# Performance work log

Hardware: AMD Instinct MI355X
Metric: run time of the kernel (lower is better)

## Reference

```python
import jax, jax.numpy as jnp
import numpy as np
from functools import partial

ITERS = 100
EPSILON = 0.8
TAU = 1.02
FEATURE_DIM = 256
MATCHED_THRESHOLD = 0.2
B, D, N0, N1 = 1, 256, 2048, 2048


def log_optimal_transport_extended(scores, alpha, iters, epsilon, tau):
    b, m, n = scores.shape
    dt = scores.dtype
    ms = jnp.asarray(m, dt)
    ns = jnp.asarray(n, dt)
    bins0 = jnp.broadcast_to(alpha, (b, m, 1)).astype(dt)
    bins1 = jnp.broadcast_to(alpha, (b, 1, n)).astype(dt)
    corner = jnp.broadcast_to(alpha, (b, 1, 1)).astype(dt)
    # couplings: [b, m+1, n+1] score matrix augmented with dustbin row/col
    couplings = jnp.concatenate([
        jnp.concatenate([scores, bins0], axis=-1),
        jnp.concatenate([bins1, corner], axis=-1)], axis=1)
    norm = -jnp.log(ms + ns)
    log_mu = jnp.concatenate([jnp.full((m,), norm, dt), (jnp.log(ns) + norm)[None]])
    log_nu = jnp.concatenate([jnp.full((n,), norm, dt), (jnp.log(ms) + norm)[None]])
    log_mu = jnp.broadcast_to(log_mu[None], (b, m + 1))
    log_nu = jnp.broadcast_to(log_nu[None], (b, n + 1))

    def step(carry, _):
        u, v = carry
        u_new = (log_mu - jax.scipy.special.logsumexp(couplings + v[:, None, :], axis=2)) / tau
        u = u + epsilon * (u_new - u)
        v_new = (log_nu - jax.scipy.special.logsumexp(couplings + u[:, :, None], axis=1)) / tau
        v = v + epsilon * (v_new - v)
        return (u, v), None

    u0 = jnp.zeros_like(log_mu)
    v0 = jnp.zeros_like(log_nu)
    (u, v), _ = jax.lax.scan(jax.checkpoint(step), (u0, v0), None, length=iters)
    Z = couplings + u[:, :, None] + v[:, None, :]
    return Z - norm


def reference(mdesc0, mdesc1, bin_score):
    # mdesc0: [b, d, n], mdesc1: [b, d, m]
    sim = jnp.einsum('bdn,bdm->bnm', mdesc0, mdesc1)
    scores = sim / np.float32(np.sqrt(FEATURE_DIM))
    Z = log_optimal_transport_extended(scores, bin_score, ITERS, EPSILON, TAU)
    inner = Z[:, :-1, :-1]                       # [b, m, n]
    m, n = inner.shape[1], inner.shape[2]
    max0_vals = inner.max(axis=2)
    indices0 = inner.argmax(axis=2)              # [b, m] int
    indices1 = inner.argmax(axis=1)              # [b, n] int
    mutual0 = jnp.arange(m)[None, :] == jnp.take_along_axis(indices1, indices0, axis=1)
    mutual1 = jnp.arange(n)[None, :] == jnp.take_along_axis(indices0, indices1, axis=1)
    zero = jnp.zeros((), inner.dtype)
    mscores0 = jnp.where(mutual0, jnp.exp(max0_vals), zero)
    mscores1 = jnp.where(mutual1, jnp.take_along_axis(mscores0, indices1, axis=1), zero)
    valid0 = mutual0 & (mscores0 > MATCHED_THRESHOLD)
    valid1 = mutual1 & jnp.take_along_axis(valid0, indices1, axis=1)
    i0 = jnp.where(valid0, indices0, -1)
    i1 = jnp.where(valid1, indices1, -1)
    return (jnp.exp(Z[0]), i0[0], i1[0], mscores0[0], mscores1[0])


def setup_inputs() -> dict:
    key = jax.random.key(0)
    k0, k1 = jax.random.split(key)
    mdesc0 = jax.random.normal(k0, (B, D, N0), dtype=jnp.float32)
    mdesc1 = jax.random.normal(k1, (B, D, N1), dtype=jnp.float32)
    bin_score = jnp.ones((), dtype=jnp.float32)  # learned dustbin score, init 1.0
    return {"mdesc0": mdesc0, "mdesc1": mdesc1, "bin_score": bin_score}
```

## Files before the change

kernel.cpp:

```cpp
#include <hip/hip_runtime.h>
#include <hip/hip_bf16.h>
#include <math.h>

#define D        256
#define NINNER   2048
#define NROW     2049
#define SP       2064
#define ITERS_N  100
#define EPS_F    0.8f
#define TAU_F    1.02f
#define NB       256
#define NT       256

typedef unsigned long long u64;

#define PSTRIDE  2112u

#define SZ_MAT   (2049u * 2064u)
#define OFF_E    0u
#define OFF_F    SZ_MAT
#define OFF_WUP  (2u * SZ_MAT)
#define OFF_WVP  (OFF_WUP + 4u * PSTRIDE)
#define OFF_MAX0 (OFF_WVP + 4u * PSTRIDE)
#define OFF_IDX0 (OFF_MAX0 + 2048u)
#define OFF_IDX1 (OFF_IDX0 + 2048u)
#define OFF_MS0  (OFF_IDX1 + 2048u)
#define OFF_VLD0 (OFF_MS0 + 2048u)

#define OOFF_Z   0u
#define OOFF_I0  (2049u * 2049u)
#define OOFF_I1  (OOFF_I0 + 2048u)
#define OOFF_S0  (OOFF_I1 + 2048u)
#define OOFF_S1  (OOFF_S0 + 2048u)

__device__ __forceinline__ float    pair_val(u64 x) { return __uint_as_float((unsigned)x); }
__device__ __forceinline__ unsigned pair_tag(u64 x) { return (unsigned)(x >> 32); }
__device__ __forceinline__ u64 make_pair(float v, unsigned t) {
    return ((u64)t << 32) | (u64)__float_as_uint(v);
}

__global__ __launch_bounds__(256) void k_gemm(const float* __restrict__ A,
                                              const float* __restrict__ Bm,
                                              float* __restrict__ E,
                                              float* __restrict__ F) {
    __shared__ float As[8][64];
    __shared__ float Bs[8][64];
    const int tid = threadIdx.x;
    const int tx = tid & 15, ty = tid >> 4;
    const int row0 = blockIdx.y * 64, col0 = blockIdx.x * 64;
    float acc[4][4] = {};
    const int lr = tid >> 6, lc = tid & 63;
    for (int k0 = 0; k0 < D; k0 += 8) {
        As[lr][lc]     = A[(k0 + lr) * NINNER + row0 + lc];
        As[lr + 4][lc] = A[(k0 + lr + 4) * NINNER + row0 + lc];
        Bs[lr][lc]     = Bm[(k0 + lr) * NINNER + col0 + lc];
        Bs[lr + 4][lc] = Bm[(k0 + lr + 4) * NINNER + col0 + lc];
        __syncthreads();
#pragma unroll
        for (int kk = 0; kk < 8; ++kk) {
            const float4 av = *(const float4*)&As[kk][ty * 4];
            const float4 bv = *(const float4*)&Bs[kk][tx * 4];
            const float a_[4] = {av.x, av.y, av.z, av.w};
            const float b_[4] = {bv.x, bv.y, bv.z, bv.w};
#pragma unroll
            for (int r = 0; r < 4; ++r)
#pragma unroll
                for (int c = 0; c < 4; ++c)
                    acc[r][c] = fmaf(a_[r], b_[c], acc[r][c]);
        }
        __syncthreads();
    }
    float o[4][4];
#pragma unroll
    for (int r = 0; r < 4; ++r)
#pragma unroll
        for (int c = 0; c < 4; ++c)
            o[r][c] = expf(acc[r][c] * 0.0625f);
    const int row = row0 + ty * 4, col = col0 + tx * 4;
#pragma unroll
    for (int r = 0; r < 4; ++r)
        *(float4*)(E + (size_t)(row + r) * SP + col)
            = make_float4(o[r][0], o[r][1], o[r][2], o[r][3]);
#pragma unroll
    for (int c = 0; c < 4; ++c)
        *(float4*)(F + (size_t)(col + c) * SP + row)
            = make_float4(o[0][c], o[1][c], o[2][c], o[3][c]);
}

__global__ __launch_bounds__(256) void k_init(float* __restrict__ E,
                                              float* __restrict__ F,
                                              u64* __restrict__ wvb0,
                                              const float* __restrict__ alpha) {
    const int t = blockIdx.x * 256 + threadIdx.x;
    const float ea = expf(alpha[0]);
    if (t < NINNER) {
        E[(size_t)t * SP + NINNER] = ea;
        F[(size_t)t * SP + NINNER] = ea;
        wvb0[t] = make_pair(1.0f, 0u);
    }
    if (t <= NINNER) {
        E[(size_t)NINNER * SP + t] = ea;
        F[(size_t)NINNER * SP + t] = ea;
    }
}

__device__ __forceinline__ void poll8(const u64* buf, int tid, unsigned want, float* w) {
    u64 a[8];
#pragma unroll
    for (int q = 0; q < 8; ++q)
        a[q] = __hip_atomic_load(buf + q * 256 + tid, __ATOMIC_RELAXED, __HIP_MEMORY_SCOPE_AGENT);
    for (;;) {
        unsigned miss = 0u;
#pragma unroll
        for (int q = 0; q < 8; ++q)
            miss |= (pair_tag(a[q]) != want) ? (1u << q) : 0u;
        if (!miss) break;
        __builtin_amdgcn_s_sleep(2);
#pragma unroll
        for (int q = 0; q < 8; ++q)
            if (miss & (1u << q))
                a[q] = __hip_atomic_load(buf + q * 256 + tid, __ATOMIC_RELAXED, __HIP_MEMORY_SCOPE_AGENT);
    }
#pragma unroll
    for (int q = 0; q < 8; ++q) w[q] = pair_val(a[q]);
}

__global__ __launch_bounds__(256, 1) void k_sinkhorn(const float* __restrict__ E,
                                                     const float* __restrict__ F,
                                                     u64* wub, u64* wvb,
                                                     const float* __restrict__ alpha) {
    const int b = blockIdx.x, tid = threadIdx.x;
    const int lane = tid & 63, wid = tid >> 6;
    const int base = b * 8;
    const bool lastb = (b == NB - 1);
    __shared__ float red[2][4][9];

    const float norm = -8.317766166719343f;
    const float logbin = 7.624618986159398f + norm;
    const float ea = expf(alpha[0]);

    float eR[8][8], fR[8][8];
#pragma unroll
    for (int r = 0; r < 8; ++r) {
        const float* rowE = E + (size_t)(base + r) * SP;
        const float* rowF = F + (size_t)(base + r) * SP;
#pragma unroll
        for (int q = 0; q < 8; ++q) {
            eR[r][q] = rowE[q * 256 + tid];
            fR[r][q] = rowF[q * 256 + tid];
        }
    }

    float u = 0.0f, v = 0.0f;
    float ub = 0.0f, vb = 0.0f;
    float eub = 1.0f, evb = 1.0f;

    for (int it = 0; it < ITERS_N; ++it) {
        {
            const u64* src = wvb + (size_t)(it & 1) * PSTRIDE;
            u64* dst = wub + (size_t)((it + 1) & 1) * PSTRIDE;
            const unsigned prod = (unsigned)(it + 1);
            float w[8];
            poll8(src, tid, (unsigned)it, w);
            float p[8];
#pragma unroll
            for (int r = 0; r < 8; ++r) {
                float s = 0.0f;
#pragma unroll
                for (int q = 0; q < 8; ++q) s = fmaf(eR[r][q], w[q], s);
                p[r] = s;
            }
            float t = w[0] + w[1] + w[2] + w[3] + w[4] + w[5] + w[6] + w[7];
#pragma unroll
            for (int r = 0; r < 8; ++r) {
                float s = p[r];
#pragma unroll
                for (int m = 1; m < 64; m <<= 1) s += __shfl_xor(s, m, 64);
                if (lane == 0) red[0][wid][r] = s;
            }
#pragma unroll
            for (int m = 1; m < 64; m <<= 1) t += __shfl_xor(t, m, 64);
            if (lane == 0) red[0][wid][8] = t;
            __syncthreads();
            const float tsum = red[0][0][8] + red[0][1][8] + red[0][2][8] + red[0][3][8];
            const float Sbin = ea * (tsum + evb);
            ub = ub + EPS_F * ((logbin - logf(Sbin)) / TAU_F - ub);
            if (tid < 8) {
                const float S = red[0][0][tid] + red[0][1][tid] + red[0][2][tid] + red[0][3][tid]
                              + ea * evb;
                const float unew = (norm - logf(S)) / TAU_F;
                u = u + EPS_F * (unew - u);
                __hip_atomic_store(dst + base + tid, make_pair(expf(u), prod),
                                   __ATOMIC_RELAXED, __HIP_MEMORY_SCOPE_AGENT);
            }
            eub = expf(ub);
        }
        {
            const u64* src = wub + (size_t)((it + 1) & 1) * PSTRIDE;
            u64* dst = wvb + (size_t)((it + 1) & 1) * PSTRIDE;
            const unsigned prod = (unsigned)(it + 1);
            float w[8];
            poll8(src, tid, prod, w);
            float p[8];
#pragma unroll
            for (int r = 0; r < 8; ++r) {
                float s = 0.0f;
#pragma unroll
                for (int q = 0; q < 8; ++q) s = fmaf(fR[r][q], w[q], s);
                p[r] = s;
            }
            float t = w[0] + w[1] + w[2] + w[3] + w[4] + w[5] + w[6] + w[7];
#pragma unroll
            for (int r = 0; r < 8; ++r) {
                float s = p[r];
#pragma unroll
                for (int m = 1; m < 64; m <<= 1) s += __shfl_xor(s, m, 64);
                if (lane == 0) red[1][wid][r] = s;
            }
#pragma unroll
            for (int m = 1; m < 64; m <<= 1) t += __shfl_xor(t, m, 64);
            if (lane == 0) red[1][wid][8] = t;
            __syncthreads();
            const float tsum = red[1][0][8] + red[1][1][8] + red[1][2][8] + red[1][3][8];
            const float Tbin = ea * (tsum + eub);
            vb = vb + EPS_F * ((logbin - logf(Tbin)) / TAU_F - vb);
            if (tid < 8) {
                const float T = red[1][0][tid] + red[1][1][tid] + red[1][2][tid] + red[1][3][tid]
                              + ea * eub;
                const float vnew = (norm - logf(T)) / TAU_F;
                v = v + EPS_F * (vnew - v);
                __hip_atomic_store(dst + base + tid, make_pair(expf(v), prod),
                                   __ATOMIC_RELAXED, __HIP_MEMORY_SCOPE_AGENT);
            }
            evb = expf(vb);
        }
    }
    if (lastb && tid == 0) {
        __hip_atomic_store(wub + NINNER, make_pair(eub, (unsigned)ITERS_N),
                           __ATOMIC_RELAXED, __HIP_MEMORY_SCOPE_AGENT);
        __hip_atomic_store(wvb + NINNER, make_pair(evb, (unsigned)ITERS_N),
                           __ATOMIC_RELAXED, __HIP_MEMORY_SCOPE_AGENT);
    }
}

__global__ __launch_bounds__(256) void k_finish(const float* __restrict__ E,
                                                const float* __restrict__ F,
                                                const float2* __restrict__ wup,
                                                const float2* __restrict__ wvp,
                                                float* __restrict__ out,
                                                float* __restrict__ max0,
                                                int* __restrict__ idx0,
                                                int* __restrict__ idx1) {
    const int i = blockIdx.x;
    const int tid = threadIdx.x;
    const int lane = tid & 63, wid = tid >> 6;
    __shared__ float sb[4]; __shared__ int si[4];

    {
        const float wui = wup[i].x * 4096.0f;
        const float* row = E + (size_t)i * SP;
        float best = -1.0f; int bidx = 0;
        for (int j = tid; j < NROW; j += 256) {
            const float val = row[j] * wvp[j].x * wui;
            out[(size_t)i * NROW + j] = val;
            if (j < NINNER && val > best) { best = val; bidx = j; }
        }
        if (i < NINNER) {
#pragma unroll
            for (int m = 1; m < 64; m <<= 1) {
                const float ob = __shfl_xor(best, m, 64);
                const int   oi = __shfl_xor(bidx, m, 64);
                if (ob > best || (ob == best && oi < bidx)) { best = ob; bidx = oi; }
            }
            if (lane == 0) { sb[wid] = best; si[wid] = bidx; }
            __syncthreads();
            if (tid == 0) {
                for (int k = 1; k < 4; ++k)
                    if (sb[k] > best || (sb[k] == best && si[k] < bidx)) { best = sb[k]; bidx = si[k]; }
                max0[i] = best; idx0[i] = bidx;
            }
        }
    }

    if (i < NINNER) {
        __syncthreads();
        const float* row = F + (size_t)i * SP;
        float best = -1.0f; int bidx = 0;
        for (int r = tid; r < NINNER; r += 256) {
            const float q = row[r] * wup[r].x;
            if (q > best) { best = q; bidx = r; }
        }
#pragma unroll
        for (int m = 1; m < 64; m <<= 1) {
            const float ob = __shfl_xor(best, m, 64);
            const int   oi = __shfl_xor(bidx, m, 64);
            if (ob > best || (ob == best && oi < bidx)) { best = ob; bidx = oi; }
        }
        if (lane == 0) { sb[wid] = best; si[wid] = bidx; }
        __syncthreads();
        if (tid == 0) {
            for (int k = 1; k < 4; ++k)
                if (sb[k] > best || (sb[k] == best && si[k] < bidx)) { best = sb[k]; bidx = si[k]; }
            idx1[i] = bidx;
        }
    }
}

__global__ __launch_bounds__(256) void k_match0(const float* __restrict__ max0,
                                                const int* __restrict__ idx0,
                                                const int* __restrict__ idx1,
                                                float* __restrict__ ms0,
                                                int* __restrict__ vld0,
                                                float* __restrict__ out) {
    const int i = blockIdx.x * 256 + threadIdx.x;
    if (i >= NINNER) return;
    const int j = idx0[i];
    const bool mut = (idx1[j] == i);
    const float ms = mut ? max0[i] : 0.0f;
    const bool val = mut && (ms > 0.2f);
    ms0[i] = ms; vld0[i] = val ? 1 : 0;
    out[OOFF_I0 + i] = val ? (float)j : -1.0f;
    out[OOFF_S0 + i] = ms;
}
__global__ __launch_bounds__(256) void k_match1(const int* __restrict__ idx0,
                                                const int* __restrict__ idx1,
                                                const float* __restrict__ ms0,
                                                const int* __restrict__ vld0,
                                                float* __restrict__ out) {
    const int j = blockIdx.x * 256 + threadIdx.x;
    if (j >= NINNER) return;
    const int i = idx1[j];
    const bool mut = (idx0[i] == j);
    const float ms = mut ? ms0[i] : 0.0f;
    const bool val = mut && (vld0[i] != 0);
    out[OOFF_I1 + j] = val ? (float)i : -1.0f;
    out[OOFF_S1 + j] = ms;
}

extern "C" void kernel_launch(void* const* d_in, const int* in_sizes, int n_in,
                              void* d_out, int out_size, void* d_ws, size_t ws_size,
                              hipStream_t stream) {
    const float* A     = (const float*)d_in[0];
    const float* Bm    = (const float*)d_in[1];
    const float* alpha = (const float*)d_in[2];

    float* ws = (float*)d_ws;
    float* E    = ws + OFF_E;
    float* F    = ws + OFF_F;
    u64*   wub  = (u64*)(ws + OFF_WUP);
    u64*   wvb  = (u64*)(ws + OFF_WVP);
    float* max0 = ws + OFF_MAX0;
    int*   idx0 = (int*)(ws + OFF_IDX0);
    int*   idx1 = (int*)(ws + OFF_IDX1);
    float* ms0  = ws + OFF_MS0;
    int*   vld0 = (int*)(ws + OFF_VLD0);
    float* out  = (float*)d_out;

    k_gemm<<<dim3(32, 32), 256, 0, stream>>>(A, Bm, E, F);
    k_init<<<dim3(16), 256, 0, stream>>>(E, F, wvb, alpha);
    k_sinkhorn<<<dim3(NB), NT, 0, stream>>>(E, F, wub, wvb, alpha);
    k_finish<<<dim3(NROW), 256, 0, stream>>>(E, F, (const float2*)wub, (const float2*)wvb,
                                             out, max0, idx0, idx1);
    k_match0<<<dim3(8), 256, 0, stream>>>(max0, idx0, idx1, ms0, vld0, out);
    k_match1<<<dim3(8), 256, 0, stream>>>(idx0, idx1, ms0, vld0, out);
}
```

Before: 901.4 us.

## Replace tagged per-element flag polling with sharded atomic counter barriers

```diff
diff --git a/kernel.cpp b/kernel.cpp
--- a/kernel.cpp
+++ b/kernel.cpp
@@ -1,5 +1,4 @@
 #include <hip/hip_runtime.h>
-#include <hip/hip_bf16.h>
 #include <math.h>
 
 #define D        256
@@ -12,32 +11,23 @@
 #define NB       256
 #define NT       256
 
-typedef unsigned long long u64;
-
-#define PSTRIDE  2112u
-
 #define SZ_MAT   (2049u * 2064u)
 #define OFF_E    0u
 #define OFF_F    SZ_MAT
-#define OFF_WUP  (2u * SZ_MAT)
-#define OFF_WVP  (OFF_WUP + 4u * PSTRIDE)
-#define OFF_MAX0 (OFF_WVP + 4u * PSTRIDE)
+#define OFF_WU   (2u * SZ_MAT)
+#define OFF_WV   (OFF_WU + 2064u)
+#define OFF_CU   (OFF_WV + 2064u)
+#define OFF_CV   (OFF_CU + 512u)
+#define OFF_MAX0 (OFF_CV + 512u)
 #define OFF_IDX0 (OFF_MAX0 + 2048u)
 #define OFF_IDX1 (OFF_IDX0 + 2048u)
 #define OFF_MS0  (OFF_IDX1 + 2048u)
 #define OFF_VLD0 (OFF_MS0 + 2048u)
 
-#define OOFF_Z   0u
 #define OOFF_I0  (2049u * 2049u)
 #define OOFF_I1  (OOFF_I0 + 2048u)
 #define OOFF_S0  (OOFF_I1 + 2048u)
 #define OOFF_S1  (OOFF_S0 + 2048u)
-
-__device__ __forceinline__ float    pair_val(u64 x) { return __uint_as_float((unsigned)x); }
-__device__ __forceinline__ unsigned pair_tag(u64 x) { return (unsigned)(x >> 32); }
-__device__ __forceinline__ u64 make_pair(float v, unsigned t) {
-    return ((u64)t << 32) | (u64)__float_as_uint(v);
-}
 
 __global__ __launch_bounds__(256) void k_gemm(const float* __restrict__ A,
                                               const float* __restrict__ Bm,
@@ -89,50 +79,37 @@
 
 __global__ __launch_bounds__(256) void k_init(float* __restrict__ E,
                                               float* __restrict__ F,
-                                              u64* __restrict__ wvb0,
+                                              float* __restrict__ wv,
+                                              unsigned* __restrict__ cu,
+                                              unsigned* __restrict__ cv,
                                               const float* __restrict__ alpha) {
     const int t = blockIdx.x * 256 + threadIdx.x;
     const float ea = expf(alpha[0]);
     if (t < NINNER) {
         E[(size_t)t * SP + NINNER] = ea;
         F[(size_t)t * SP + NINNER] = ea;
-        wvb0[t] = make_pair(1.0f, 0u);
+        wv[t] = 1.0f;
     }
     if (t <= NINNER) {
         E[(size_t)NINNER * SP + t] = ea;
         F[(size_t)NINNER * SP + t] = ea;
     }
-}
-
-__device__ __forceinline__ void poll8(const u64* buf, int tid, unsigned want, float* w) {
-    u64 a[8];
-#pragma unroll
-    for (int q = 0; q < 8; ++q)
-        a[q] = __hip_atomic_load(buf + q * 256 + tid, __ATOMIC_RELAXED, __HIP_MEMORY_SCOPE_AGENT);
-    for (;;) {
-        unsigned miss = 0u;
-#pragma unroll
-        for (int q = 0; q < 8; ++q)
-            miss |= (pair_tag(a[q]) != want) ? (1u << q) : 0u;
-        if (!miss) break;
-        __builtin_amdgcn_s_sleep(2);
-#pragma unroll
-        for (int q = 0; q < 8; ++q)
-            if (miss & (1u << q))
-                a[q] = __hip_atomic_load(buf + q * 256 + tid, __ATOMIC_RELAXED, __HIP_MEMORY_SCOPE_AGENT);
-    }
-#pragma unroll
-    for (int q = 0; q < 8; ++q) w[q] = pair_val(a[q]);
+    if (t < 8) {
+        cu[t * 64] = 0u;
+        cv[t * 64] = NB / 8;
+    }
 }
 
 __global__ __launch_bounds__(256, 1) void k_sinkhorn(const float* __restrict__ E,
                                                      const float* __restrict__ F,
-                                                     u64* wub, u64* wvb,
+                                                     float* __restrict__ wu,
+                                                     float* __restrict__ wv,
+                                                     unsigned* __restrict__ cu,
+                                                     unsigned* __restrict__ cv,
                                                      const float* __restrict__ alpha) {
     const int b = blockIdx.x, tid = threadIdx.x;
     const int lane = tid & 63, wid = tid >> 6;
     const int base = b * 8;
-    const bool lastb = (b == NB - 1);
     __shared__ float red[2][4][9];
 
     const float norm = -8.317766166719343f;
@@ -156,12 +133,25 @@
     float eub = 1.0f, evb = 1.0f;
 
     for (int it = 0; it < ITERS_N; ++it) {
+        const unsigned tgt = (unsigned)(NB * (it + 1));
         {
-            const u64* src = wvb + (size_t)(it & 1) * PSTRIDE;
-            u64* dst = wub + (size_t)((it + 1) & 1) * PSTRIDE;
-            const unsigned prod = (unsigned)(it + 1);
+            if (tid == 0) {
+                for (;;) {
+                    unsigned s = 0;
+#pragma unroll
+                    for (int k = 0; k < 8; ++k)
+                        s += __hip_atomic_load(cv + k * 64, __ATOMIC_RELAXED,
+                                               __HIP_MEMORY_SCOPE_AGENT);
+                    if (s >= tgt) break;
+                    __builtin_amdgcn_s_sleep(1);
+                }
+            }
+            __syncthreads();
             float w[8];
-            poll8(src, tid, (unsigned)it, w);
+#pragma unroll
+            for (int q = 0; q < 8; ++q)
+                w[q] = __hip_atomic_load(wv + q * 256 + tid, __ATOMIC_RELAXED,
+                                         __HIP_MEMORY_SCOPE_AGENT);
             float p[8];
 #pragma unroll
             for (int r = 0; r < 8; ++r) {
@@ -190,17 +180,32 @@
                               + ea * evb;
                 const float unew = (norm - logf(S)) / TAU_F;
                 u = u + EPS_F * (unew - u);
-                __hip_atomic_store(dst + base + tid, make_pair(expf(u), prod),
+                __hip_atomic_store(wu + base + tid, expf(u),
                                    __ATOMIC_RELAXED, __HIP_MEMORY_SCOPE_AGENT);
             }
+            if (tid == 0)
+                __hip_atomic_fetch_add(cu + (b & 7) * 64, 1u,
+                                       __ATOMIC_RELEASE, __HIP_MEMORY_SCOPE_AGENT);
             eub = expf(ub);
         }
         {
-            const u64* src = wub + (size_t)((it + 1) & 1) * PSTRIDE;
-            u64* dst = wvb + (size_t)((it + 1) & 1) * PSTRIDE;
-            const unsigned prod = (unsigned)(it + 1);
+            if (tid == 0) {
+                for (;;) {
+                    unsigned s = 0;
+#pragma unroll
+                    for (int k = 0; k < 8; ++k)
+                        s += __hip_atomic_load(cu + k * 64, __ATOMIC_RELAXED,
+                                               __HIP_MEMORY_SCOPE_AGENT);
+                    if (s >= tgt) break;
+                    __builtin_amdgcn_s_sleep(1);
+                }
+            }
+            __syncthreads();
             float w[8];
-            poll8(src, tid, prod, w);
+#pragma unroll
+            for (int q = 0; q < 8; ++q)
+                w[q] = __hip_atomic_load(wu + q * 256 + tid, __ATOMIC_RELAXED,
+                                         __HIP_MEMORY_SCOPE_AGENT);
             float p[8];
 #pragma unroll
             for (int r = 0; r < 8; ++r) {
@@ -229,24 +234,25 @@
                               + ea * eub;
                 const float vnew = (norm - logf(T)) / TAU_F;
                 v = v + EPS_F * (vnew - v);
-                __hip_atomic_store(dst + base + tid, make_pair(expf(v), prod),
+                __hip_atomic_store(wv + base + tid, expf(v),
                                    __ATOMIC_RELAXED, __HIP_MEMORY_SCOPE_AGENT);
             }
+            if (tid == 0)
+                __hip_atomic_fetch_add(cv + (b & 7) * 64, 1u,
+                                       __ATOMIC_RELEASE, __HIP_MEMORY_SCOPE_AGENT);
             evb = expf(vb);
         }
     }
-    if (lastb && tid == 0) {
-        __hip_atomic_store(wub + NINNER, make_pair(eub, (unsigned)ITERS_N),
-                           __ATOMIC_RELAXED, __HIP_MEMORY_SCOPE_AGENT);
-        __hip_atomic_store(wvb + NINNER, make_pair(evb, (unsigned)ITERS_N),
-                           __ATOMIC_RELAXED, __HIP_MEMORY_SCOPE_AGENT);
+    if (b == NB - 1 && tid == 0) {
+        wu[NINNER] = eub;
+        wv[NINNER] = evb;
     }
 }
 
 __global__ __launch_bounds__(256) void k_finish(const float* __restrict__ E,
                                                 const float* __restrict__ F,
-                                                const float2* __restrict__ wup,
-                                                const float2* __restrict__ wvp,
+                                                const float* __restrict__ wu,
+                                                const float* __restrict__ wv,
                                                 float* __restrict__ out,
                                                 float* __restrict__ max0,
                                                 int* __restrict__ idx0,
@@ -257,11 +263,11 @@
     __shared__ float sb[4]; __shared__ int si[4];
 
     {
-        const float wui = wup[i].x * 4096.0f;
+        const float wui = wu[i] * 4096.0f;
         const float* row = E + (size_t)i * SP;
         float best = -1.0f; int bidx = 0;
         for (int j = tid; j < NROW; j += 256) {
-            const float val = row[j] * wvp[j].x * wui;
+            const float val = row[j] * wv[j] * wui;
             out[(size_t)i * NROW + j] = val;
             if (j < NINNER && val > best) { best = val; bidx = j; }
         }
@@ -287,7 +293,7 @@
         const float* row = F + (size_t)i * SP;
         float best = -1.0f; int bidx = 0;
         for (int r = tid; r < NINNER; r += 256) {
-            const float q = row[r] * wup[r].x;
+            const float q = row[r] * wu[r];
             if (q > best) { best = q; bidx = r; }
         }
 #pragma unroll
@@ -345,22 +351,23 @@
     const float* alpha = (const float*)d_in[2];
 
     float* ws = (float*)d_ws;
-    float* E    = ws + OFF_E;
-    float* F    = ws + OFF_F;
-    u64*   wub  = (u64*)(ws + OFF_WUP);
-    u64*   wvb  = (u64*)(ws + OFF_WVP);
-    float* max0 = ws + OFF_MAX0;
-    int*   idx0 = (int*)(ws + OFF_IDX0);
-    int*   idx1 = (int*)(ws + OFF_IDX1);
-    float* ms0  = ws + OFF_MS0;
-    int*   vld0 = (int*)(ws + OFF_VLD0);
-    float* out  = (float*)d_out;
+    float* E      = ws + OFF_E;
+    float* F      = ws + OFF_F;
+    float* wu     = ws + OFF_WU;
+    float* wv     = ws + OFF_WV;
+    unsigned* cu  = (unsigned*)(ws + OFF_CU);
+    unsigned* cv  = (unsigned*)(ws + OFF_CV);
+    float* max0   = ws + OFF_MAX0;
+    int*   idx0   = (int*)(ws + OFF_IDX0);
+    int*   idx1   = (int*)(ws + OFF_IDX1);
+    float* ms0    = ws + OFF_MS0;
+    int*   vld0   = (int*)(ws + OFF_VLD0);
+    float* out    = (float*)d_out;
 
     k_gemm<<<dim3(32, 32), 256, 0, stream>>>(A, Bm, E, F);
-    k_init<<<dim3(16), 256, 0, stream>>>(E, F, wvb, alpha);
-    k_sinkhorn<<<dim3(NB), NT, 0, stream>>>(E, F, wub, wvb, alpha);
-    k_finish<<<dim3(NROW), 256, 0, stream>>>(E, F, (const float2*)wub, (const float2*)wvb,
-                                             out, max0, idx0, idx1);
+    k_init<<<dim3(16), 256, 0, stream>>>(E, F, wv, cu, cv, alpha);
+    k_sinkhorn<<<dim3(NB), NT, 0, stream>>>(E, F, wu, wv, cu, cv, alpha);
+    k_finish<<<dim3(NROW), 256, 0, stream>>>(E, F, wu, wv, out, max0, idx0, idx1);
     k_match0<<<dim3(8), 256, 0, stream>>>(max0, idx0, idx1, ms0, vld0, out);
     k_match1<<<dim3(8), 256, 0, stream>>>(idx0, idx1, ms0, vld0, out);
 }
```

Measured after the change: 1.244 ms. +38.0%, slower.

## Halve Sinkhorn block count with 16 rows per block and vectorized polling

Applied to the files above, without the earlier changes.

```diff
diff --git a/kernel.cpp b/kernel.cpp
--- a/kernel.cpp
+++ b/kernel.cpp
@@ -1,5 +1,4 @@
 #include <hip/hip_runtime.h>
-#include <hip/hip_bf16.h>
 #include <math.h>
 
 #define D        256
@@ -9,10 +8,12 @@
 #define ITERS_N  100
 #define EPS_F    0.8f
 #define TAU_F    1.02f
-#define NB       256
-#define NT       256
+#define NB_S     128
+#define NT_S     512
+#define ROWS     16
 
 typedef unsigned long long u64;
+typedef __attribute__((ext_vector_type(4))) unsigned int uint4v;
 
 #define PSTRIDE  2112u
 
@@ -27,7 +28,6 @@
 #define OFF_MS0  (OFF_IDX1 + 2048u)
 #define OFF_VLD0 (OFF_MS0 + 2048u)
 
-#define OOFF_Z   0u
 #define OOFF_I0  (2049u * 2049u)
 #define OOFF_I1  (OOFF_I0 + 2048u)
 #define OOFF_S0  (OOFF_I1 + 2048u)
@@ -104,51 +104,45 @@
     }
 }
 
-__device__ __forceinline__ void poll8(const u64* buf, int tid, unsigned want, float* w) {
-    u64 a[8];
-#pragma unroll
-    for (int q = 0; q < 8; ++q)
-        a[q] = __hip_atomic_load(buf + q * 256 + tid, __ATOMIC_RELAXED, __HIP_MEMORY_SCOPE_AGENT);
+__device__ __forceinline__ void poll4(const u64* buf, int tid, unsigned want, float* w) {
+    const u64* p = buf + 4 * (size_t)tid;
+    uint4v x, y;
     for (;;) {
-        unsigned miss = 0u;
-#pragma unroll
-        for (int q = 0; q < 8; ++q)
-            miss |= (pair_tag(a[q]) != want) ? (1u << q) : 0u;
-        if (!miss) break;
-        __builtin_amdgcn_s_sleep(2);
-#pragma unroll
-        for (int q = 0; q < 8; ++q)
-            if (miss & (1u << q))
-                a[q] = __hip_atomic_load(buf + q * 256 + tid, __ATOMIC_RELAXED, __HIP_MEMORY_SCOPE_AGENT);
-    }
-#pragma unroll
-    for (int q = 0; q < 8; ++q) w[q] = pair_val(a[q]);
-}
-
-__global__ __launch_bounds__(256, 1) void k_sinkhorn(const float* __restrict__ E,
+        asm volatile("global_load_dwordx4 %0, %2, off sc0 sc1\n\t"
+                     "global_load_dwordx4 %1, %2, off offset:16 sc0 sc1\n\t"
+                     "s_waitcnt vmcnt(0)"
+                     : "=&v"(x), "=&v"(y)
+                     : "v"(p)
+                     : "memory");
+        if (x.y == want && x.w == want && y.y == want && y.w == want) break;
+        __builtin_amdgcn_s_sleep(1);
+    }
+    __builtin_amdgcn_sched_barrier(0);
+    w[0] = __uint_as_float(x.x); w[1] = __uint_as_float(x.z);
+    w[2] = __uint_as_float(y.x); w[3] = __uint_as_float(y.z);
+}
+
+__global__ __launch_bounds__(512, 2) void k_sinkhorn(const float* __restrict__ E,
                                                      const float* __restrict__ F,
                                                      u64* wub, u64* wvb,
                                                      const float* __restrict__ alpha) {
     const int b = blockIdx.x, tid = threadIdx.x;
     const int lane = tid & 63, wid = tid >> 6;
-    const int base = b * 8;
-    const bool lastb = (b == NB - 1);
-    __shared__ float red[2][4][9];
+    const int base = b * ROWS;
+    const bool lastb = (b == NB_S - 1);
+    __shared__ float red[2][8][17];
 
     const float norm = -8.317766166719343f;
     const float logbin = 7.624618986159398f + norm;
     const float ea = expf(alpha[0]);
 
-    float eR[8][8], fR[8][8];
-#pragma unroll
-    for (int r = 0; r < 8; ++r) {
-        const float* rowE = E + (size_t)(base + r) * SP;
-        const float* rowF = F + (size_t)(base + r) * SP;
-#pragma unroll
-        for (int q = 0; q < 8; ++q) {
-            eR[r][q] = rowE[q * 256 + tid];
-            fR[r][q] = rowF[q * 256 + tid];
-        }
+    float eR[ROWS][4], fR[ROWS][4];
+#pragma unroll
+    for (int r = 0; r < ROWS; ++r) {
+        const float4 ev = *(const float4*)(E + (size_t)(base + r) * SP + 4 * tid);
+        const float4 fv = *(const float4*)(F + (size_t)(base + r) * SP + 4 * tid);
+        eR[r][0] = ev.x; eR[r][1] = ev.y; eR[r][2] = ev.z; eR[r][3] = ev.w;
+        fR[r][0] = fv.x; fR[r][1] = fv.y; fR[r][2] = fv.z; fR[r][3] = fv.w;
     }
 
     float u = 0.0f, v = 0.0f;
@@ -160,19 +154,19 @@
             const u64* src = wvb + (size_t)(it & 1) * PSTRIDE;
             u64* dst = wub + (size_t)((it + 1) & 1) * PSTRIDE;
             const unsigned prod = (unsigned)(it + 1);
-            float w[8];
-            poll8(src, tid, (unsigned)it, w);
-            float p[8];
-#pragma unroll
-            for (int r = 0; r < 8; ++r) {
+            float w[4];
+            poll4(src, tid, (unsigned)it, w);
+            float p[ROWS];
+#pragma unroll
+            for (int r = 0; r < ROWS; ++r) {
                 float s = 0.0f;
 #pragma unroll
-                for (int q = 0; q < 8; ++q) s = fmaf(eR[r][q], w[q], s);
+                for (int q = 0; q < 4; ++q) s = fmaf(eR[r][q], w[q], s);
                 p[r] = s;
             }
-            float t = w[0] + w[1] + w[2] + w[3] + w[4] + w[5] + w[6] + w[7];
-#pragma unroll
-            for (int r = 0; r < 8; ++r) {
+            float t = w[0] + w[1] + w[2] + w[3];
+#pragma unroll
+            for (int r = 0; r < ROWS; ++r) {
                 float s = p[r];
 #pragma unroll
                 for (int m = 1; m < 64; m <<= 1) s += __shfl_xor(s, m, 64);
@@ -180,14 +174,17 @@
             }
 #pragma unroll
             for (int m = 1; m < 64; m <<= 1) t += __shfl_xor(t, m, 64);
-            if (lane == 0) red[0][wid][8] = t;
+            if (lane == 0) red[0][wid][16] = t;
             __syncthreads();
-            const float tsum = red[0][0][8] + red[0][1][8] + red[0][2][8] + red[0][3][8];
+            float tsum = 0.0f;
+#pragma unroll
+            for (int k = 0; k < 8; ++k) tsum += red[0][k][16];
             const float Sbin = ea * (tsum + evb);
             ub = ub + EPS_F * ((logbin - logf(Sbin)) / TAU_F - ub);
-            if (tid < 8) {
-                const float S = red[0][0][tid] + red[0][1][tid] + red[0][2][tid] + red[0][3][tid]
-                              + ea * evb;
+            if (tid < ROWS) {
+                float S = ea * evb;
+#pragma unroll
+                for (int k = 0; k < 8; ++k) S += red[0][k][tid];
                 const float unew = (norm - logf(S)) / TAU_F;
                 u = u + EPS_F * (unew - u);
                 __hip_atomic_store(dst + base + tid, make_pair(expf(u), prod),
@@ -199,19 +196,19 @@
             const u64* src = wub + (size_t)((it + 1) & 1) * PSTRIDE;
             u64* dst = wvb + (size_t)((it + 1) & 1) * PSTRIDE;
             const unsigned prod = (unsigned)(it + 1);
-            float w[8];
-            poll8(src, tid, prod, w);
-            float p[8];
-#pragma unroll
-            for (int r = 0; r < 8; ++r) {
+            float w[4];
+            poll4(src, tid, prod, w);
+            float p[ROWS];
+#pragma unroll
+            for (int r = 0; r < ROWS; ++r) {
                 float s = 0.0f;
 #pragma unroll
-                for (int q = 0; q < 8; ++q) s = fmaf(fR[r][q], w[q], s);
+                for (int q = 0; q < 4; ++q) s = fmaf(fR[r][q], w[q], s);
                 p[r] = s;
             }
-            float t = w[0] + w[1] + w[2] + w[3] + w[4] + w[5] + w[6] + w[7];
-#pragma unroll
-            for (int r = 0; r < 8; ++r) {
+            float t = w[0] + w[1] + w[2] + w[3];
+#pragma unroll
+            for (int r = 0; r < ROWS; ++r) {
                 float s = p[r];
 #pragma unroll
                 for (int m = 1; m < 64; m <<= 1) s += __shfl_xor(s, m, 64);
@@ -219,14 +216,17 @@
             }
 #pragma unroll
             for (int m = 1; m < 64; m <<= 1) t += __shfl_xor(t, m, 64);
-            if (lane == 0) red[1][wid][8] = t;
+            if (lane == 0) red[1][wid][16] = t;
             __syncthreads();
-            const float tsum = red[1][0][8] + red[1][1][8] + red[1][2][8] + red[1][3][8];
+            float tsum = 0.0f;
+#pragma unroll
+            for (int k = 0; k < 8; ++k) tsum += red[1][k][16];
             const float Tbin = ea * (tsum + eub);
             vb = vb + EPS_F * ((logbin - logf(Tbin)) / TAU_F - vb);
-            if (tid < 8) {
-                const float T = red[1][0][tid] + red[1][1][tid] + red[1][2][tid] + red[1][3][tid]
-                              + ea * eub;
+            if (tid < ROWS) {
+                float T = ea * eub;
+#pragma unroll
+                for (int k = 0; k < 8; ++k) T += red[1][k][tid];
                 const float vnew = (norm - logf(T)) / TAU_F;
                 v = v + EPS_F * (vnew - v);
                 __hip_atomic_store(dst + base + tid, make_pair(expf(v), prod),
@@ -358,7 +358,7 @@
 
     k_gemm<<<dim3(32, 32), 256, 0, stream>>>(A, Bm, E, F);
     k_init<<<dim3(16), 256, 0, stream>>>(E, F, wvb, alpha);
-    k_sinkhorn<<<dim3(NB), NT, 0, stream>>>(E, F, wub, wvb, alpha);
+    k_sinkhorn<<<dim3(NB_S), NT_S, 0, stream>>>(E, F, wub, wvb, alpha);
     k_finish<<<dim3(NROW), 256, 0, stream>>>(E, F, (const float2*)wub, (const float2*)wvb,
                                              out, max0, idx0, idx1);
     k_match0<<<dim3(8), 256, 0, stream>>>(max0, idx0, idx1, ms0, vld0, out);
```

Measured after the change: 1.140 ms. 26.5% more time.
